# Optimization experiments

Measured on AMD Instinct MI355X. Metric: run time of the kernel, lower is better.

Reference implementation:

```python
import jax, jax.numpy as jnp
import numpy as np

BQ = 64  # query block size
BK = 64  # key block size
PV_SCALE = 1e-3  # pvthreshd (~0..50) -> prob threshold, mirrors int8 P-quantization cutoff


def setup_inputs() -> dict:
    key = jax.random.key(0)
    ks = jax.random.split(key, 6)
    B, H, L, D = 2, 16, 2048, 64
    q = jax.random.normal(ks[0], (B, H, L, D), jnp.float32)
    k = jax.random.normal(ks[1], (B, H, L, D), jnp.float32)
    v = jax.random.normal(ks[2], (B, H, L, D), jnp.float32)
    # per-head tuned thresholds (init defaults / autotune ranges)
    cdfthreshd = 0.85 + 0.14 * jax.random.uniform(ks[3], (H,), jnp.float32)
    simthreshd1 = jax.random.uniform(ks[4], (H,), jnp.float32, minval=-0.3, maxval=0.5)
    pvthreshd = jax.random.uniform(ks[5], (H,), jnp.float32, minval=15.0, maxval=25.0)
    return dict(q=q, k=k, v=v, cdfthreshd=cdfthreshd,
                simthreshd1=simthreshd1, pvthreshd=pvthreshd)


def _sparse_meansim_attention(q, k, v, cdfthreshd, simthreshd1, pvthreshd):
    B, H, L, D = q.shape
    nqb, nkb = L // BQ, L // BK
    scale = 1.0 / jnp.sqrt(jnp.float32(D))

    # smooth_k: subtract per-(B,H) key mean along sequence
    k = k - k.mean(axis=2, keepdims=True)

    qb = q.reshape(B, H, nqb, BQ, D)
    kb = k.reshape(B, H, nkb, BK, D)
    qm = qb.mean(axis=3)  # [B,H,nqb,D]
    km = kb.mean(axis=3)  # [B,H,nkb,D]

    # mean cosine similarity of queries to their block mean -> pooled (prunable) blocks
    qn = jnp.linalg.norm(qb, axis=-1)            # [B,H,nqb,BQ]
    qmn = jnp.linalg.norm(qm, axis=-1)           # [B,H,nqb]
    cos = jnp.einsum('bhnqd,bhnd->bhnq', qb, qm) / (qn * qmn[..., None] + 1e-6)
    pooled = cos.mean(axis=-1) > simthreshd1[None, :, None]  # [B,H,nqb]

    # block-level score map from pooled means, CDF-based top-mass block selection
    s = jnp.einsum('bhid,bhjd->bhij', qm, km) * scale        # [B,H,nqb,nkb]
    p = jax.nn.softmax(s, axis=-1)
    order = jnp.argsort(-p, axis=-1)
    p_sorted = jnp.take_along_axis(p, order, axis=-1)
    excl_cdf = jnp.cumsum(p_sorted, axis=-1) - p_sorted      # exclusive CDF
    keep_sorted = excl_cdf < cdfthreshd[None, :, None, None]
    keep = jnp.take_along_axis(keep_sorted, jnp.argsort(order, axis=-1), axis=-1)

    sink = (jnp.arange(nkb) == 0)  # attention_sink: always keep first key block
    block_mask = keep | (~pooled)[..., None] | sink          # [B,H,nqb,nkb]

    # full attention restricted to selected blocks
    S = jnp.einsum('bhqd,bhkd->bhqk', q, k) * scale          # [B,H,L,L]
    m = jnp.repeat(jnp.repeat(block_mask, BQ, axis=2), BK, axis=3)
    P = jax.nn.softmax(jnp.where(m, S, -jnp.inf), axis=-1)

    # second-stage PV pruning: skip PV accumulation for negligible prob blocks
    Pb = P.reshape(B, H, nqb, BQ, nkb, BK)
    pv_keep = Pb.max(axis=(3, 5)) >= pvthreshd[None, :, None, None] * PV_SCALE
    pv_keep = pv_keep | sink
    Pb = Pb * pv_keep[:, :, :, None, :, None].astype(P.dtype)

    o = jnp.einsum('bhqk,bhkd->bhqd', Pb.reshape(B, H, L, L), v)
    return o


def reference(q, k, v, cdfthreshd, simthreshd1, pvthreshd):
    return _sparse_meansim_attention(q, k, v, cdfthreshd, simthreshd1, pvthreshd)
```

## Files before the change

kernel.cpp:

```cpp
#include <hip/hip_runtime.h>
#include <hip/hip_bf16.h>
#include <math.h>
#include <stdint.h>

#define B 2
#define H 16
#define L 2048
#define D 64
#define NB 32
#define PTS 72

typedef unsigned short u16;
typedef unsigned int u32;
typedef __attribute__((ext_vector_type(2))) unsigned int u32x2;
typedef __attribute__((ext_vector_type(4))) unsigned int u32x4;
typedef __attribute__((ext_vector_type(8))) short s16x8;
typedef __attribute__((ext_vector_type(4))) float f32x4;

union FragU { s16x8 v; u32 u[4]; };

__device__ __forceinline__ u32 pkbf(float a, float b) {
  __hip_bfloat162 h = __float22bfloat162_rn(make_float2(a, b));
  union { __hip_bfloat162 h; u32 u; } cv; cv.h = h; return cv.u;
}
__device__ __forceinline__ float bf2f(u32 u16bits) {
  union { u32 u; float f; } c; c.u = u16bits << 16; return c.f;
}
__device__ __forceinline__ void split4(float4 p, u32x2& hi, u32x2& lo) {
  u32 h01 = pkbf(p.x, p.y), h23 = pkbf(p.z, p.w);
  float rx = p.x - bf2f(h01 & 0xffffu);
  float ry = p.y - bf2f(h01 >> 16);
  float rz = p.z - bf2f(h23 & 0xffffu);
  float rw = p.w - bf2f(h23 >> 16);
  hi = (u32x2){h01, h23};
  lo = (u32x2){pkbf(rx, ry), pkbf(rz, rw)};
}

__global__ __launch_bounds__(256) void k_prep(const float* __restrict__ k,
                                              const float* __restrict__ v,
                                              float* __restrict__ ksum,
                                              u16* __restrict__ khi_g,
                                              u16* __restrict__ klo_g,
                                              u16* __restrict__ vthi_g,
                                              u16* __restrict__ vtlo_g,
                                              float* __restrict__ kbmax) {
  int blk = blockIdx.x, bh = blk >> 5, j = blk & 31, t = threadIdx.x;
  int lane = t & 63, w = t >> 6;
  __shared__ float vt[64 * 65];
  __shared__ float pk_[4][64];
  __shared__ unsigned bmaxS;
  if (t == 0) bmaxS = 0u;
  size_t base = (size_t)blk * 4096;

  int r0 = t >> 3;
  int c8 = (t & 7) * 8;
  float cs[8] = {0.f, 0.f, 0.f, 0.f, 0.f, 0.f, 0.f, 0.f};
  float rmax = 0.f;
#pragma unroll
  for (int it = 0; it < 2; ++it) {
    int r = r0 + 32 * it;
    const float* kp = k + base + r * 64 + c8;
    float4 f0 = *(const float4*)kp;
    float4 f1 = *(const float4*)(kp + 4);
    u32x2 h0, l0, h1, l1;
    split4(f0, h0, l0); split4(f1, h1, l1);
    *(u32x4*)(khi_g + base + r * 64 + c8) = (u32x4){h0[0], h0[1], h1[0], h1[1]};
    *(u32x4*)(klo_g + base + r * 64 + c8) = (u32x4){l0[0], l0[1], l1[0], l1[1]};
    cs[0] += f0.x; cs[1] += f0.y; cs[2] += f0.z; cs[3] += f0.w;
    cs[4] += f1.x; cs[5] += f1.y; cs[6] += f1.z; cs[7] += f1.w;
    float ssq = f0.x*f0.x + f0.y*f0.y + f0.z*f0.z + f0.w*f0.w
              + f1.x*f1.x + f1.y*f1.y + f1.z*f1.z + f1.w*f1.w;
    ssq += __shfl_xor(ssq, 1); ssq += __shfl_xor(ssq, 2); ssq += __shfl_xor(ssq, 4);
    if ((t & 7) == 0) rmax = fmaxf(rmax, ssq);
    const float* vp = v + base + r * 64 + c8;
    float4 g0 = *(const float4*)vp;
    float4 g1 = *(const float4*)(vp + 4);
    vt[(c8 + 0) * 65 + r] = g0.x;
    vt[(c8 + 1) * 65 + r] = g0.y;
    vt[(c8 + 2) * 65 + r] = g0.z;
    vt[(c8 + 3) * 65 + r] = g0.w;
    vt[(c8 + 4) * 65 + r] = g1.x;
    vt[(c8 + 5) * 65 + r] = g1.y;
    vt[(c8 + 6) * 65 + r] = g1.z;
    vt[(c8 + 7) * 65 + r] = g1.w;
  }
  if ((t & 7) == 0) atomicMax(&bmaxS, __float_as_uint(rmax));
#pragma unroll
  for (int i = 0; i < 8; ++i) {
    cs[i] += __shfl_xor(cs[i], 8);
    cs[i] += __shfl_xor(cs[i], 16);
    cs[i] += __shfl_xor(cs[i], 32);
  }
  if (lane < 8) {
    *(float4*)&pk_[w][lane * 8]     = (float4){cs[0], cs[1], cs[2], cs[3]};
    *(float4*)&pk_[w][lane * 8 + 4] = (float4){cs[4], cs[5], cs[6], cs[7]};
  }
  __syncthreads();
  if (t < 64) ksum[(size_t)blk * 64 + t] = pk_[0][t] + pk_[1][t] + pk_[2][t] + pk_[3][t];
  if (t == 0) kbmax[blk] = __uint_as_float(bmaxS);
#pragma unroll
  for (int it = 0; it < 2; ++it) {
    int idx = t + 256 * it, d = idx >> 3, s8 = (idx & 7) * 8;
    const float* vr = &vt[d * 65 + s8];
    float4 f0 = {vr[0], vr[1], vr[2], vr[3]};
    float4 f1 = {vr[4], vr[5], vr[6], vr[7]};
    u32x2 h0, l0, h1, l1;
    split4(f0, h0, l0); split4(f1, h1, l1);
    size_t o = (size_t)bh * 131072 + (size_t)d * 2048 + j * 64 + s8;
    *(u32x4*)(vthi_g + o) = (u32x4){h0[0], h0[1], h1[0], h1[1]};
    *(u32x4*)(vtlo_g + o) = (u32x4){l0[0], l0[1], l1[0], l1[1]};
  }
}

__global__ __launch_bounds__(256, 4) void k_attn(
    const float* __restrict__ q,
    const float* __restrict__ ksum,
    const u16* __restrict__ khi_g, const u16* __restrict__ klo_g,
    const u16* __restrict__ vthi_g, const u16* __restrict__ vtlo_g,
    const float* __restrict__ cdfthreshd, const float* __restrict__ simthreshd1,
    const float* __restrict__ pvthreshd, const float* __restrict__ kbmax,
    float* __restrict__ out) {
  int blk0 = blockIdx.x;
  int blk = (blk0 & 7) * 128 + (blk0 >> 3);
  int bh = blk >> 5, iq = blk & 31, h = bh & (H - 1);
  int t = threadIdx.x, lane = t & 63, w = t >> 6;
  int m16 = lane & 15, quad = lane >> 4;

  __shared__ __align__(16) uint8_t smem[36896];
  u16*   pbase = (u16*)smem;
  u32*   rbm   = (u32*)smem;
  float* lpart = (float*)(smem + 8448);
  float* qmS   = (float*)(smem + 9472);
  float* MSs   = (float*)(smem + 9728);
  float* linvS = (float*)(smem + 9984);
  int*   flg   = (int*)(smem + 36864);
#define PHB(b) (pbase + (b) * 9216)
#define PLB(b) (pbase + (b) * 9216 + 4608)

  const float* qg = q + ((size_t)bh * L + (size_t)iq * 64) * D;
  const u16* kh = khi_g + (size_t)bh * (L * D);
  const u16* kl = klo_g + (size_t)bh * (L * D);
  const u16* vh = vthi_g + (size_t)bh * (L * D);
  const u16* vl = vtlo_g + (size_t)bh * (L * D);

  s16x8 qhf[4][2], qlf[4][2];
#pragma unroll
  for (int nt = 0; nt < 4; ++nt)
#pragma unroll
    for (int ks = 0; ks < 2; ++ks) {
      const float* p0 = qg + (size_t)(16 * nt + m16) * 64 + ks * 32 + quad * 8;
      float4 a = *(const float4*)p0;
      float4 b2 = *(const float4*)(p0 + 4);
      u32x2 ha, la, hb, lb;
      split4(a, ha, la); split4(b2, hb, lb);
      FragU fh, fl;
      fh.u[0] = ha[0]; fh.u[1] = ha[1]; fh.u[2] = hb[0]; fh.u[3] = hb[1];
      fl.u[0] = la[0]; fl.u[1] = la[1]; fl.u[2] = lb[0]; fl.u[3] = lb[1];
      qhf[nt][ks] = fh.v; qlf[nt][ks] = fl.v;
    }
  for (int e = t; e < 64 * 33; e += 256) rbm[e] = 0x7F800000u;

  if (w == 0) {
    float s = 0.f;
    for (int r = 0; r < 64; ++r) s += qg[r * 64 + lane];
    qmS[lane] = s * (1.f / 64.f);
  }
  if (w == 1) {
    float m = (lane < 32) ? kbmax[bh * 32 + lane] : 0.f;
    for (int off = 16; off; off >>= 1) m = fmaxf(m, __shfl_xor(m, off, 32));
    if (lane == 0) ((float*)flg)[3] = m;
  }
  __syncthreads();

  bool keepj = false;
  if (w == 0 && lane < 32) {
    int j = lane;
    const float* ksp = ksum + (size_t)bh * NB * 64 + j * 64;
    float sv = 0.f;
    for (int d = 0; d < 64; ++d) sv += qmS[d] * ksp[d];
    sv *= (1.f / 64.f) * 0.125f;
    float mx = sv;
    for (int off = 16; off; off >>= 1) mx = fmaxf(mx, __shfl_xor(mx, off, 32));
    float p = expf(sv - mx);
    float sum = p;
    for (int off = 16; off; off >>= 1) sum += __shfl_xor(sum, off, 32);
    p /= sum;
    float excl = 0.f;
    for (int u = 0; u < 32; ++u) {
      float pu = __shfl(p, u, 32);
      if ((pu > p) || (pu == p && u < j)) excl += pu;
    }
    keepj = excl < cdfthreshd[h];
  }
  if (w == 1) {
    int r = lane;
    float kmax2 = ((float*)flg)[3];
    float dot = 0.f, qn2 = 0.f, qmn2 = 0.f;
    for (int d = 0; d < 64; ++d) {
      float a = qg[r * 64 + d], b2 = qmS[d];
      dot += a * b2; qn2 += a * a; qmn2 += b2 * b2;
    }
    float cs = dot / (sqrtf(qn2) * sqrtf(qmn2) + 1e-6f);
    float su = cs;
    for (int off = 32; off; off >>= 1) su += __shfl_xor(su, off);
    if (lane == 0) flg[0] = (su * (1.f / 64.f)) > simthreshd1[h];
    MSs[r] = sqrtf(qn2 * kmax2) * 0.125f;
  }
  __syncthreads();
  if (w == 0 && lane < 32) {
    bool bit = keepj || !flg[0] || (lane == 0);
    unsigned long long bal = __ballot(bit);
    if (lane == 0) flg[1] = (int)(u32)bal;
  }
  __syncthreads();
  u32 mw = (u32)flg[1];

  float Mq[4];
#pragma unroll
  for (int nt = 0; nt < 4; ++nt) Mq[nt] = MSs[16 * nt + m16];

  float lp[4] = {0.f, 0.f, 0.f, 0.f};
  {
    u32 rm = mw;
    while (rm) {
      int j = (int)__builtin_ctz(rm); rm &= rm - 1;
      s16x8 ka[2][2];
      const u16* kr0 = kh + (size_t)(j * 64 + 16 * w + m16) * 64 + quad * 8;
      const u16* kl0 = kl + (size_t)(j * 64 + 16 * w + m16) * 64 + quad * 8;
#pragma unroll
      for (int ks = 0; ks < 2; ++ks) {
        ka[ks][0] = *(const s16x8*)(kr0 + ks * 32);
        ka[ks][1] = *(const s16x8*)(kl0 + ks * 32);
      }
      f32x4 acc[4];
#pragma unroll
      for (int nt = 0; nt < 4; ++nt) acc[nt] = (f32x4){0.f, 0.f, 0.f, 0.f};
      __builtin_amdgcn_s_setprio(1);
#pragma unroll
      for (int ks = 0; ks < 2; ++ks)
#pragma unroll
        for (int nt = 0; nt < 4; ++nt) {
          acc[nt] = __builtin_amdgcn_mfma_f32_16x16x32_bf16(ka[ks][0], qhf[nt][ks], acc[nt], 0, 0, 0);
          acc[nt] = __builtin_amdgcn_mfma_f32_16x16x32_bf16(ka[ks][1], qhf[nt][ks], acc[nt], 0, 0, 0);
          acc[nt] = __builtin_amdgcn_mfma_f32_16x16x32_bf16(ka[ks][0], qlf[nt][ks], acc[nt], 0, 0, 0);
        }
      __builtin_amdgcn_s_setprio(0);
#pragma unroll
      for (int nt = 0; nt < 4; ++nt) {
        float vmax = -1e30f;
#pragma unroll
        for (int reg = 0; reg < 4; ++reg) {
          float s = acc[nt][reg] * 0.125f - Mq[nt];
          lp[nt] += __expf(s);
          vmax = fmaxf(vmax, s);
        }
        vmax = fmaxf(vmax, __shfl_xor(vmax, 16));
        vmax = fmaxf(vmax, __shfl_xor(vmax, 32));
        if (quad == 0)
          atomicMin(rbm + (16 * nt + m16) * 33 + j, __float_as_uint(fmaxf(-vmax, 0.f)));
      }
    }
  }
#pragma unroll
  for (int nt = 0; nt < 4; ++nt) {
    float s = lp[nt];
    s += __shfl_xor(s, 16); s += __shfl_xor(s, 32);
    if (quad == 0) lpart[w * 64 + 16 * nt + m16] = s;
  }
  __syncthreads();
  if (t < 64) linvS[t] = 1.f / (lpart[t] + lpart[64 + t] + lpart[128 + t] + lpart[192 + t]);
  __syncthreads();

  if (w == 0 && lane < 32) {
    bool keep = (mw >> lane) & 1u;
    if (keep && lane != 0) {
      float thr = pvthreshd[h] * 1e-3f;
      float mp = 0.f;
      for (int r = 0; r < 64; ++r) {
        float key = __uint_as_float(rbm[r * 33 + lane]);
        mp = fmaxf(mp, __expf(-key) * linvS[r]);
      }
      keep = mp >= thr;
    }
    unsigned long long bal = __ballot(keep);
    if (lane == 0) flg[2] = (int)(u32)bal;
  }
  __syncthreads();
  u32 gm = (u32)flg[2];

  float linq[4];
#pragma unroll
  for (int nt = 0; nt < 4; ++nt) linq[nt] = linvS[16 * nt + m16];
  __syncthreads();

  f32x4 oacc[4];
#pragma unroll
  for (int nt = 0; nt < 4; ++nt) oacc[nt] = (f32x4){0.f, 0.f, 0.f, 0.f};
  {
    u32 rg = gm;
    int buf = 0;
    while (rg) {
      int j = (int)__builtin_ctz(rg); rg &= rg - 1;
      s16x8 ka[2][2];
      const u16* kr0 = kh + (size_t)(j * 64 + 16 * w + m16) * 64 + quad * 8;
      const u16* kl0 = kl + (size_t)(j * 64 + 16 * w + m16) * 64 + quad * 8;
#pragma unroll
      for (int ks = 0; ks < 2; ++ks) {
        ka[ks][0] = *(const s16x8*)(kr0 + ks * 32);
        ka[ks][1] = *(const s16x8*)(kl0 + ks * 32);
      }
      f32x4 acc[4];
#pragma unroll
      for (int nt = 0; nt < 4; ++nt) acc[nt] = (f32x4){0.f, 0.f, 0.f, 0.f};
      __builtin_amdgcn_s_setprio(1);
#pragma unroll
      for (int ks = 0; ks < 2; ++ks)
#pragma unroll
        for (int nt = 0; nt < 4; ++nt) {
          acc[nt] = __builtin_amdgcn_mfma_f32_16x16x32_bf16(ka[ks][0], qhf[nt][ks], acc[nt], 0, 0, 0);
          acc[nt] = __builtin_amdgcn_mfma_f32_16x16x32_bf16(ka[ks][1], qhf[nt][ks], acc[nt], 0, 0, 0);
          acc[nt] = __builtin_amdgcn_mfma_f32_16x16x32_bf16(ka[ks][0], qlf[nt][ks], acc[nt], 0, 0, 0);
        }
      __builtin_amdgcn_s_setprio(0);
      u16* ph = PHB(buf);
      u16* pl = PLB(buf);
#pragma unroll
      for (int nt = 0; nt < 4; ++nt) {
        float4 pv;
        pv.x = __expf(acc[nt][0] * 0.125f - Mq[nt]) * linq[nt];
        pv.y = __expf(acc[nt][1] * 0.125f - Mq[nt]) * linq[nt];
        pv.z = __expf(acc[nt][2] * 0.125f - Mq[nt]) * linq[nt];
        pv.w = __expf(acc[nt][3] * 0.125f - Mq[nt]) * linq[nt];
        u32x2 hi, lo; split4(pv, hi, lo);
        int off = (16 * nt + m16) * PTS + 16 * w + 4 * quad;
        *(u32x2*)(ph + off) = hi;
        *(u32x2*)(pl + off) = lo;
      }
      __syncthreads();
      s16x8 va[2][2];
      const u16* vr0 = vh + (size_t)(16 * w + m16) * L + j * 64 + quad * 8;
      const u16* vl0 = vl + (size_t)(16 * w + m16) * L + j * 64 + quad * 8;
#pragma unroll
      for (int ks = 0; ks < 2; ++ks) {
        va[ks][0] = *(const s16x8*)(vr0 + ks * 32);
        va[ks][1] = *(const s16x8*)(vl0 + ks * 32);
      }
#pragma unroll
      for (int ks = 0; ks < 2; ++ks)
#pragma unroll
        for (int nt = 0; nt < 4; ++nt) {
          s16x8 pbh = *(const s16x8*)(ph + (16 * nt + m16) * PTS + ks * 32 + quad * 8);
          s16x8 pbl = *(const s16x8*)(pl + (16 * nt + m16) * PTS + ks * 32 + quad * 8);
          __builtin_amdgcn_s_setprio(1);
          oacc[nt] = __builtin_amdgcn_mfma_f32_16x16x32_bf16(va[ks][0], pbh, oacc[nt], 0, 0, 0);
          oacc[nt] = __builtin_amdgcn_mfma_f32_16x16x32_bf16(va[ks][1], pbh, oacc[nt], 0, 0, 0);
          oacc[nt] = __builtin_amdgcn_mfma_f32_16x16x32_bf16(va[ks][0], pbl, oacc[nt], 0, 0, 0);
          __builtin_amdgcn_s_setprio(0);
        }
      buf ^= 1;
    }
  }

  float* ob = out + ((size_t)bh * L + (size_t)iq * 64) * D;
#pragma unroll
  for (int nt = 0; nt < 4; ++nt)
    *(f32x4*)(ob + (size_t)(16 * nt + m16) * 64 + 16 * w + 4 * quad) = oacc[nt];
}

extern "C" void kernel_launch(void* const* d_in, const int* in_sizes, int n_in,
                              void* d_out, int out_size, void* d_ws, size_t ws_size,
                              hipStream_t stream) {
  (void)in_sizes; (void)n_in; (void)out_size; (void)ws_size;
  const float* q   = (const float*)d_in[0];
  const float* k   = (const float*)d_in[1];
  const float* v   = (const float*)d_in[2];
  const float* cdf = (const float*)d_in[3];
  const float* sim = (const float*)d_in[4];
  const float* pvt = (const float*)d_in[5];
  float* out = (float*)d_out;

  uint8_t* w8 = (uint8_t*)d_ws;
  float* ksum  = (float*)w8;
  float* kbmax = (float*)(w8 + 262144);
  u16* khi_g  = (u16*)(w8 + 266240);
  u16* klo_g  = khi_g + (size_t)B * H * L * D;
  u16* vthi_g = klo_g + (size_t)B * H * L * D;
  u16* vtlo_g = vthi_g + (size_t)B * H * L * D;

  k_prep<<<B * H * NB, 256, 0, stream>>>(k, v, ksum, khi_g, klo_g, vthi_g, vtlo_g, kbmax);
  k_attn<<<B * H * NB, 256, 0, stream>>>(q, ksum, khi_g, klo_g, vthi_g, vtlo_g,
                                         cdf, sim, pvt, kbmax, out);
}
```

Measured before the change: 239.1 us.

## Prefetch next K block, move Q-lo fragments to LDS, single-buffer P

```diff
diff --git a/kernel.cpp b/kernel.cpp
--- a/kernel.cpp
+++ b/kernel.cpp
@@ -126,16 +126,17 @@
   int t = threadIdx.x, lane = t & 63, w = t >> 6;
   int m16 = lane & 15, quad = lane >> 4;
 
-  __shared__ __align__(16) uint8_t smem[36896];
+  __shared__ __align__(16) uint8_t smem[27680];
   u16*   pbase = (u16*)smem;
   u32*   rbm   = (u32*)smem;
   float* lpart = (float*)(smem + 8448);
   float* qmS   = (float*)(smem + 9472);
   float* MSs   = (float*)(smem + 9728);
   float* linvS = (float*)(smem + 9984);
-  int*   flg   = (int*)(smem + 36864);
-#define PHB(b) (pbase + (b) * 9216)
-#define PLB(b) (pbase + (b) * 9216 + 4608)
+  u16*   qlo   = (u16*)(smem + 18432);
+  int*   flg   = (int*)(smem + 27648);
+  u16* PH = pbase;
+  u16* PL = pbase + 4608;
 
   const float* qg = q + ((size_t)bh * L + (size_t)iq * 64) * D;
   const u16* kh = khi_g + (size_t)bh * (L * D);
@@ -143,7 +144,7 @@
   const u16* vh = vthi_g + (size_t)bh * (L * D);
   const u16* vl = vtlo_g + (size_t)bh * (L * D);
 
-  s16x8 qhf[4][2], qlf[4][2];
+  s16x8 qhf[4][2];
 #pragma unroll
   for (int nt = 0; nt < 4; ++nt)
 #pragma unroll
@@ -153,10 +154,11 @@
       float4 b2 = *(const float4*)(p0 + 4);
       u32x2 ha, la, hb, lb;
       split4(a, ha, la); split4(b2, hb, lb);
-      FragU fh, fl;
+      FragU fh;
       fh.u[0] = ha[0]; fh.u[1] = ha[1]; fh.u[2] = hb[0]; fh.u[3] = hb[1];
-      fl.u[0] = la[0]; fl.u[1] = la[1]; fl.u[2] = lb[0]; fl.u[3] = lb[1];
-      qhf[nt][ks] = fh.v; qlf[nt][ks] = fl.v;
+      qhf[nt][ks] = fh.v;
+      *(u32x4*)(qlo + (16 * nt + m16) * PTS + ks * 32 + quad * 8) =
+          (u32x4){la[0], la[1], lb[0], lb[1]};
     }
   for (int e = t; e < 64 * 33; e += 256) rbm[e] = 0x7F800000u;
 
@@ -222,29 +224,48 @@
   float lp[4] = {0.f, 0.f, 0.f, 0.f};
   {
     u32 rm = mw;
-    while (rm) {
-      int j = (int)__builtin_ctz(rm); rm &= rm - 1;
-      s16x8 ka[2][2];
+    int j = (int)__builtin_ctz(rm); rm &= rm - 1;
+    s16x8 ka0[2], ka1[2];
+    {
       const u16* kr0 = kh + (size_t)(j * 64 + 16 * w + m16) * 64 + quad * 8;
       const u16* kl0 = kl + (size_t)(j * 64 + 16 * w + m16) * 64 + quad * 8;
 #pragma unroll
       for (int ks = 0; ks < 2; ++ks) {
-        ka[ks][0] = *(const s16x8*)(kr0 + ks * 32);
-        ka[ks][1] = *(const s16x8*)(kl0 + ks * 32);
-      }
+        ka0[ks] = *(const s16x8*)(kr0 + ks * 32);
+        ka1[ks] = *(const s16x8*)(kl0 + ks * 32);
+      }
+    }
+    for (;;) {
       f32x4 acc[4];
 #pragma unroll
       for (int nt = 0; nt < 4; ++nt) acc[nt] = (f32x4){0.f, 0.f, 0.f, 0.f};
-      __builtin_amdgcn_s_setprio(1);
-#pragma unroll
-      for (int ks = 0; ks < 2; ++ks)
+#pragma unroll
+      for (int ks = 0; ks < 2; ++ks) {
+        s16x8 ql_[4];
+#pragma unroll
+        for (int nt = 0; nt < 4; ++nt)
+          ql_[nt] = *(const s16x8*)(qlo + (16 * nt + m16) * PTS + ks * 32 + quad * 8);
+        __builtin_amdgcn_s_setprio(1);
 #pragma unroll
         for (int nt = 0; nt < 4; ++nt) {
-          acc[nt] = __builtin_amdgcn_mfma_f32_16x16x32_bf16(ka[ks][0], qhf[nt][ks], acc[nt], 0, 0, 0);
-          acc[nt] = __builtin_amdgcn_mfma_f32_16x16x32_bf16(ka[ks][1], qhf[nt][ks], acc[nt], 0, 0, 0);
-          acc[nt] = __builtin_amdgcn_mfma_f32_16x16x32_bf16(ka[ks][0], qlf[nt][ks], acc[nt], 0, 0, 0);
-        }
-      __builtin_amdgcn_s_setprio(0);
+          acc[nt] = __builtin_amdgcn_mfma_f32_16x16x32_bf16(ka0[ks], qhf[nt][ks], acc[nt], 0, 0, 0);
+          acc[nt] = __builtin_amdgcn_mfma_f32_16x16x32_bf16(ka1[ks], qhf[nt][ks], acc[nt], 0, 0, 0);
+          acc[nt] = __builtin_amdgcn_mfma_f32_16x16x32_bf16(ka0[ks], ql_[nt], acc[nt], 0, 0, 0);
+        }
+        __builtin_amdgcn_s_setprio(0);
+      }
+      int nj = -1;
+      s16x8 kn0[2], kn1[2];
+      if (rm) {
+        nj = (int)__builtin_ctz(rm); rm &= rm - 1;
+        const u16* nr = kh + (size_t)(nj * 64 + 16 * w + m16) * 64 + quad * 8;
+        const u16* nl = kl + (size_t)(nj * 64 + 16 * w + m16) * 64 + quad * 8;
+#pragma unroll
+        for (int ks = 0; ks < 2; ++ks) {
+          kn0[ks] = *(const s16x8*)(nr + ks * 32);
+          kn1[ks] = *(const s16x8*)(nl + ks * 32);
+        }
+      }
 #pragma unroll
       for (int nt = 0; nt < 4; ++nt) {
         float vmax = -1e30f;
@@ -259,6 +280,10 @@
         if (quad == 0)
           atomicMin(rbm + (16 * nt + m16) * 33 + j, __float_as_uint(fmaxf(-vmax, 0.f)));
       }
+      if (nj < 0) break;
+#pragma unroll
+      for (int ks = 0; ks < 2; ++ks) { ka0[ks] = kn0[ks]; ka1[ks] = kn1[ks]; }
+      j = nj;
     }
   }
 #pragma unroll
@@ -291,39 +316,55 @@
   float linq[4];
 #pragma unroll
   for (int nt = 0; nt < 4; ++nt) linq[nt] = linvS[16 * nt + m16];
-  __syncthreads();
 
   f32x4 oacc[4];
 #pragma unroll
   for (int nt = 0; nt < 4; ++nt) oacc[nt] = (f32x4){0.f, 0.f, 0.f, 0.f};
   {
     u32 rg = gm;
-    int buf = 0;
-    while (rg) {
-      int j = (int)__builtin_ctz(rg); rg &= rg - 1;
-      s16x8 ka[2][2];
+    int j = (int)__builtin_ctz(rg); rg &= rg - 1;
+    s16x8 ka0[2], ka1[2];
+    {
       const u16* kr0 = kh + (size_t)(j * 64 + 16 * w + m16) * 64 + quad * 8;
       const u16* kl0 = kl + (size_t)(j * 64 + 16 * w + m16) * 64 + quad * 8;
 #pragma unroll
       for (int ks = 0; ks < 2; ++ks) {
-        ka[ks][0] = *(const s16x8*)(kr0 + ks * 32);
-        ka[ks][1] = *(const s16x8*)(kl0 + ks * 32);
-      }
+        ka0[ks] = *(const s16x8*)(kr0 + ks * 32);
+        ka1[ks] = *(const s16x8*)(kl0 + ks * 32);
+      }
+    }
+    for (;;) {
       f32x4 acc[4];
 #pragma unroll
       for (int nt = 0; nt < 4; ++nt) acc[nt] = (f32x4){0.f, 0.f, 0.f, 0.f};
-      __builtin_amdgcn_s_setprio(1);
-#pragma unroll
-      for (int ks = 0; ks < 2; ++ks)
+#pragma unroll
+      for (int ks = 0; ks < 2; ++ks) {
+        s16x8 ql_[4];
+#pragma unroll
+        for (int nt = 0; nt < 4; ++nt)
+          ql_[nt] = *(const s16x8*)(qlo + (16 * nt + m16) * PTS + ks * 32 + quad * 8);
+        __builtin_amdgcn_s_setprio(1);
 #pragma unroll
         for (int nt = 0; nt < 4; ++nt) {
-          acc[nt] = __builtin_amdgcn_mfma_f32_16x16x32_bf16(ka[ks][0], qhf[nt][ks], acc[nt], 0, 0, 0);
-          acc[nt] = __builtin_amdgcn_mfma_f32_16x16x32_bf16(ka[ks][1], qhf[nt][ks], acc[nt], 0, 0, 0);
-          acc[nt] = __builtin_amdgcn_mfma_f32_16x16x32_bf16(ka[ks][0], qlf[nt][ks], acc[nt], 0, 0, 0);
-        }
-      __builtin_amdgcn_s_setprio(0);
-      u16* ph = PHB(buf);
-      u16* pl = PLB(buf);
+          acc[nt] = __builtin_amdgcn_mfma_f32_16x16x32_bf16(ka0[ks], qhf[nt][ks], acc[nt], 0, 0, 0);
+          acc[nt] = __builtin_amdgcn_mfma_f32_16x16x32_bf16(ka1[ks], qhf[nt][ks], acc[nt], 0, 0, 0);
+          acc[nt] = __builtin_amdgcn_mfma_f32_16x16x32_bf16(ka0[ks], ql_[nt], acc[nt], 0, 0, 0);
+        }
+        __builtin_amdgcn_s_setprio(0);
+      }
+      int nj = -1;
+      s16x8 kn0[2], kn1[2];
+      if (rg) {
+        nj = (int)__builtin_ctz(rg); rg &= rg - 1;
+        const u16* nr = kh + (size_t)(nj * 64 + 16 * w + m16) * 64 + quad * 8;
+        const u16* nl = kl + (size_t)(nj * 64 + 16 * w + m16) * 64 + quad * 8;
+#pragma unroll
+        for (int ks = 0; ks < 2; ++ks) {
+          kn0[ks] = *(const s16x8*)(nr + ks * 32);
+          kn1[ks] = *(const s16x8*)(nl + ks * 32);
+        }
+      }
+      __syncthreads();
 #pragma unroll
       for (int nt = 0; nt < 4; ++nt) {
         float4 pv;
@@ -333,31 +374,36 @@
         pv.w = __expf(acc[nt][3] * 0.125f - Mq[nt]) * linq[nt];
         u32x2 hi, lo; split4(pv, hi, lo);
         int off = (16 * nt + m16) * PTS + 16 * w + 4 * quad;
-        *(u32x2*)(ph + off) = hi;
-        *(u32x2*)(pl + off) = lo;
+        *(u32x2*)(PH + off) = hi;
+        *(u32x2*)(PL + off) = lo;
+      }
+      s16x8 va0[2], va1[2];
+      {
+        const u16* vr0 = vh + (size_t)(16 * w + m16) * L + j * 64 + quad * 8;
+        const u16* vl0 = vl + (size_t)(16 * w + m16) * L + j * 64 + quad * 8;
+#pragma unroll
+        for (int ks = 0; ks < 2; ++ks) {
+          va0[ks] = *(const s16x8*)(vr0 + ks * 32);
+          va1[ks] = *(const s16x8*)(vl0 + ks * 32);
+        }
       }
       __syncthreads();
-      s16x8 va[2][2];
-      const u16* vr0 = vh + (size_t)(16 * w + m16) * L + j * 64 + quad * 8;
-      const u16* vl0 = vl + (size_t)(16 * w + m16) * L + j * 64 + quad * 8;
-#pragma unroll
-      for (int ks = 0; ks < 2; ++ks) {
-        va[ks][0] = *(const s16x8*)(vr0 + ks * 32);
-        va[ks][1] = *(const s16x8*)(vl0 + ks * 32);
-      }
 #pragma unroll
       for (int ks = 0; ks < 2; ++ks)
 #pragma unroll
         for (int nt = 0; nt < 4; ++nt) {
-          s16x8 pbh = *(const s16x8*)(ph + (16 * nt + m16) * PTS + ks * 32 + quad * 8);
-          s16x8 pbl = *(const s16x8*)(pl + (16 * nt + m16) * PTS + ks * 32 + quad * 8);
+          s16x8 pbh = *(const s16x8*)(PH + (16 * nt + m16) * PTS + ks * 32 + quad * 8);
+          s16x8 pbl = *(const s16x8*)(PL + (16 * nt + m16) * PTS + ks * 32 + quad * 8);
           __builtin_amdgcn_s_setprio(1);
-          oacc[nt] = __builtin_amdgcn_mfma_f32_16x16x32_bf16(va[ks][0], pbh, oacc[nt], 0, 0, 0);
-          oacc[nt] = __builtin_amdgcn_mfma_f32_16x16x32_bf16(va[ks][1], pbh, oacc[nt], 0, 0, 0);
-          oacc[nt] = __builtin_amdgcn_mfma_f32_16x16x32_bf16(va[ks][0], pbl, oacc[nt], 0, 0, 0);
+          oacc[nt] = __builtin_amdgcn_mfma_f32_16x16x32_bf16(va0[ks], pbh, oacc[nt], 0, 0, 0);
+          oacc[nt] = __builtin_amdgcn_mfma_f32_16x16x32_bf16(va1[ks], pbh, oacc[nt], 0, 0, 0);
+          oacc[nt] = __builtin_amdgcn_mfma_f32_16x16x32_bf16(va0[ks], pbl, oacc[nt], 0, 0, 0);
           __builtin_amdgcn_s_setprio(0);
         }
-      buf ^= 1;
+      if (nj < 0) break;
+#pragma unroll
+      for (int ks = 0; ks < 2; ++ks) { ka0[ks] = kn0[ks]; ka1[ks] = kn1[ks]; }
+      j = nj;
     }
   }
 
```

Result: faster. 231.4 us (-3.2%).
